# Kernel tuning notes

Measured on AMD Instinct MI355X. Metric: run time of the kernel, lower is better.

## Reference

```python
import jax, jax.numpy as jnp
import numpy as np

EPS = 1e-6  # torch F.cosine_similarity eps


def setup_inputs() -> dict:
    key = jax.random.key(0)
    k1, = jax.random.split(key, 1)
    N, M, D = 1024, 10, 768
    dvecs = jax.random.normal(k1, (N, M, D), dtype=jnp.float32)
    w = jnp.full((1,), 10.0, dtype=jnp.float32)   # init_w
    b = jnp.full((1,), -5.0, dtype=jnp.float32)   # init_b
    return {"dvecs": dvecs, "w": w, "b": b}


def _ge2e_softmax_loss(dvecs, w, b):
    N, M, D = dvecs.shape
    sums = jnp.sum(dvecs, axis=1)                      # (N, D)
    ctrds = sums / M                                   # full centroids
    excl = (sums[:, None, :] - dvecs) / (M - 1)        # (N, M, D) leave-one-out centroids

    dnorm = jnp.maximum(jnp.linalg.norm(dvecs, axis=-1), EPS)   # (N, M)
    cnorm = jnp.maximum(jnp.linalg.norm(ctrds, axis=-1), EPS)   # (N,)
    enorm = jnp.maximum(jnp.linalg.norm(excl, axis=-1), EPS)    # (N, M)

    # cosine sim of every utterance to every full centroid: (N, M, N)
    sim_all = jnp.einsum('nmd,kd->nmk', dvecs, ctrds) / (dnorm[:, :, None] * cnorm[None, None, :])
    # cosine sim of each utterance to its own excluded centroid: (N, M)
    sim_own = jnp.sum(dvecs * excl, axis=-1) / (dnorm * enorm)

    own_mask = jnp.eye(N, dtype=bool)[:, None, :]      # (N, 1, N)
    sim = jnp.where(own_mask, sim_own[:, :, None], sim_all)

    sim = sim * w[0] + b[0]
    losses = -jax.nn.log_softmax(sim, axis=2)          # (N, M, N)
    # pick entry [s, u, s] for each utterance
    own = jnp.take_along_axis(losses, jnp.broadcast_to(jnp.arange(N)[:, None, None], (N, M, 1)), axis=2)
    return jnp.sum(own)


def reference(dvecs, w, b):
    return _ge2e_softmax_loss(dvecs, w, b)
```

## Files before the change

### kernel.cpp

```cpp
#include <hip/hip_runtime.h>
#include <hip/hip_bf16.h>

#define EPS 1e-6f

typedef __attribute__((ext_vector_type(4))) float f32x4;

__device__ inline unsigned int pack_fp8x4(float x, float y, float z, float w) {
  int r = 0;
  r = __builtin_amdgcn_cvt_pk_fp8_f32(x, y, r, false);
  r = __builtin_amdgcn_cvt_pk_fp8_f32(z, w, r, true);
  return (unsigned int)r;
}

__global__ void __launch_bounds__(192) ge2e_pre(
    const float* __restrict__ dv, unsigned int* __restrict__ a8u,
    unsigned int* __restrict__ c8u, float* __restrict__ simown,
    float* __restrict__ rowsum, float* __restrict__ out) {
  const int n = blockIdx.x, t = threadIdx.x;
  if (n == 0 && t == 0) out[0] = 0.f;
  const float* base = dv + (size_t)n * 7680;
  float4 v[10];
  float4 s4 = make_float4(0.f, 0.f, 0.f, 0.f);
#pragma unroll
  for (int m = 0; m < 10; ++m) {
    v[m] = *reinterpret_cast<const float4*>(&base[m * 768 + 4 * t]);
    s4.x += v[m].x; s4.y += v[m].y; s4.z += v[m].z; s4.w += v[m].w;
  }
  float part[21];
#pragma unroll
  for (int m = 0; m < 10; ++m) {
    part[m]      = v[m].x * s4.x + v[m].y * s4.y + v[m].z * s4.z + v[m].w * s4.w;
    part[10 + m] = v[m].x * v[m].x + v[m].y * v[m].y + v[m].z * v[m].z + v[m].w * v[m].w;
  }
  part[20] = s4.x * s4.x + s4.y * s4.y + s4.z * s4.z + s4.w * s4.w;
#pragma unroll
  for (int k = 0; k < 21; ++k) {
#pragma unroll
    for (int off = 32; off >= 1; off >>= 1) part[k] += __shfl_xor(part[k], off);
  }
  __shared__ float red[3][21];
  __shared__ float bc[21];
  const int lane = t & 63, wid = t >> 6;
  if (lane == 0) {
#pragma unroll
    for (int k = 0; k < 21; ++k) red[wid][k] = part[k];
  }
  __syncthreads();
  if (t < 21) bc[t] = red[0][t] + red[1][t] + red[2][t];
  __syncthreads();
  const float ss = bc[20];
  const float rc = 1.0f / fmaxf(sqrtf(ss), 10.0f * EPS);
  c8u[n * 192 + t] = pack_fp8x4(s4.x * rc, s4.y * rc, s4.z * rc, s4.w * rc);
#pragma unroll
  for (int m = 0; m < 10; ++m) {
    float rd = 1.0f / fmaxf(sqrtf(bc[10 + m]), EPS);
    a8u[(size_t)(n * 10 + m) * 192 + t] =
        pack_fp8x4(v[m].x * rd, v[m].y * rd, v[m].z * rd, v[m].w * rd);
  }
  if (t < 10) {
    float dot = bc[t], sq = bc[10 + t];
    float dn = fmaxf(sqrtf(sq), EPS);
    float en = fmaxf(sqrtf(fmaxf(ss - 2.f * dot + sq, 0.f)) * (1.0f / 9.0f), EPS);
    simown[n * 10 + t] = ((dot - sq) * (1.0f / 9.0f)) / (dn * en);
    rowsum[n * 10 + t] = 0.f;
  }
}

__global__ void __launch_bounds__(256, 3) ge2e_gemm(
    const unsigned char* __restrict__ a8, const unsigned char* __restrict__ c8,
    const float* __restrict__ simown, const float* __restrict__ wp,
    float* __restrict__ rowsum) {
  __shared__ unsigned char As[2][2][128 * 32];
  __shared__ unsigned char Bs[2][2][128 * 32];
  const int t = threadIdx.x;
  const int lane = t & 63, wid = t >> 6;
  const int bx = blockIdx.x;
  const int wg = (bx & 7) * 80 + (bx >> 3);
  const int rb = wg >> 3, cb = wg & 7;
  const int row0 = rb * 128, col0 = cb * 128;
  const int wr = wid >> 1, wc = wid & 1;
  const int l15 = lane & 15, lg = lane >> 4;

  f32x4 acc[4][4];
#pragma unroll
  for (int i = 0; i < 4; ++i)
#pragma unroll
    for (int j = 0; j < 4; ++j) acc[i][j] = (f32x4){0.f, 0.f, 0.f, 0.f};

  auto STAGE = [&](int buf, int kk) {
#pragma unroll
    for (int jj = 0; jj < 2; ++jj) {
      const int s = wid * 2 + jj;
      const int c = s * 64 + lane;
      const int half = c >> 8, row = (c >> 1) & 127, k16 = c & 1;
      const unsigned char* srcA =
          a8 + (size_t)(row0 + row) * 768 + kk + half * 32 + k16 * 16;
      unsigned char* dstA = &As[buf][0][0] + s * 1024;
      __builtin_amdgcn_global_load_lds(
          (const __attribute__((address_space(1))) unsigned int*)srcA,
          (__attribute__((address_space(3))) unsigned int*)dstA, 16, 0, 0);
      const unsigned char* srcB =
          c8 + (size_t)(col0 + row) * 768 + kk + half * 32 + k16 * 16;
      unsigned char* dstB = &Bs[buf][0][0] + s * 1024;
      __builtin_amdgcn_global_load_lds(
          (const __attribute__((address_space(1))) unsigned int*)srcB,
          (__attribute__((address_space(3))) unsigned int*)dstB, 16, 0, 0);
    }
  };
  auto COMPUTE = [&](int buf) {
    long long af[4][2], bq[4][2];
#pragma unroll
    for (int i = 0; i < 4; ++i)
#pragma unroll
      for (int h = 0; h < 2; ++h)
        af[i][h] = *(const long long*)&As[buf][h][(wr * 64 + i * 16 + l15) * 32 + lg * 8];
#pragma unroll
    for (int j = 0; j < 4; ++j)
#pragma unroll
      for (int h = 0; h < 2; ++h)
        bq[j][h] = *(const long long*)&Bs[buf][h][(wc * 64 + j * 16 + l15) * 32 + lg * 8];
#pragma unroll
    for (int h = 0; h < 2; ++h)
#pragma unroll
      for (int i = 0; i < 4; ++i)
#pragma unroll
        for (int j = 0; j < 4; ++j)
          acc[i][j] = __builtin_amdgcn_mfma_f32_16x16x32_fp8_fp8(
              af[i][h], bq[j][h], acc[i][j], 0, 0, 0);
  };

  STAGE(0, 0);
  asm volatile("s_waitcnt vmcnt(0)" ::: "memory");
  __builtin_amdgcn_s_barrier();
  int cur = 0;
  for (int tt = 0; tt < 11; ++tt) {
    STAGE(cur ^ 1, (tt + 1) * 64);
    COMPUTE(cur);
    asm volatile("s_waitcnt vmcnt(0)" ::: "memory");
    __builtin_amdgcn_s_barrier();
    cur ^= 1;
  }
  COMPUTE(cur);

  const float wv = wp[0];
  const int R0 = row0 + wr * 64, C0 = col0 + wc * 64;
#pragma unroll
  for (int i = 0; i < 4; ++i) {
#pragma unroll
    for (int r = 0; r < 4; ++r) {
      const int grow = R0 + i * 16 + lg * 4 + r;
      const int ownc = grow / 10;
      float sm = 0.f;
#pragma unroll
      for (int j = 0; j < 4; ++j) {
        const int gcol = C0 + j * 16 + l15;
        float vv = wv * acc[i][j][r];
        if (gcol == ownc) vv = wv * simown[grow];
        sm += __expf(vv);
      }
#pragma unroll
      for (int off = 1; off < 16; off <<= 1) sm += __shfl_xor(sm, off, 16);
      if (l15 == 0) atomicAdd(&rowsum[grow], sm);
    }
  }
}

__global__ void __launch_bounds__(256) ge2e_final(
    const float* __restrict__ rowsum, const float* __restrict__ simown,
    const float* __restrict__ wp, float* __restrict__ out) {
  const int i = blockIdx.x * 256 + threadIdx.x;
  const float wv = wp[0];
  float loss = logf(rowsum[i]) - wv * simown[i];
#pragma unroll
  for (int off = 32; off >= 1; off >>= 1) loss += __shfl_xor(loss, off);
  __shared__ float red[4];
  const int lane = threadIdx.x & 63, wid = threadIdx.x >> 6;
  if (lane == 0) red[wid] = loss;
  __syncthreads();
  if (threadIdx.x == 0) atomicAdd(out, red[0] + red[1] + red[2] + red[3]);
}

extern "C" void kernel_launch(void* const* d_in, const int* in_sizes, int n_in,
                              void* d_out, int out_size, void* d_ws, size_t ws_size,
                              hipStream_t stream) {
  (void)in_sizes; (void)n_in; (void)out_size; (void)ws_size;
  const float* dv = (const float*)d_in[0];
  const float* wp = (const float*)d_in[1];

  unsigned char* a8 = (unsigned char*)d_ws;
  unsigned char* c8 = (unsigned char*)d_ws + 7864320;
  float* simown = (float*)((char*)d_ws + 8650752);
  float* rowsum = (float*)((char*)d_ws + 8691712);
  float* out = (float*)d_out;

  ge2e_pre<<<1024, 192, 0, stream>>>(dv, (unsigned int*)a8, (unsigned int*)c8,
                                     simown, rowsum, out);
  ge2e_gemm<<<640, 256, 0, stream>>>(a8, c8, simown, wp, rowsum);
  ge2e_final<<<40, 256, 0, stream>>>(rowsum, simown, wp, out);
}
```

Measured before the change: 47.36 us.

## Use 256x256 GEMM tiles with 8 waves, LDS swizzle, and interleaved staging

Grows the fp8 GEMM tile from 128x128 to 256x256 using 512-thread blocks (8 waves, each computing 128x64), cutting the grid to 160 blocks. An XOR swizzle on the LDS layout is meant to reduce bank conflicts. Loads for the next K-tile are split into half-steps interleaved with the MFMA groups, using partial vmcnt waits and setprio. This gives more data reuse per block, but 160 blocks may underfill the 256 CUs and each thread now holds more accumulators.

```diff
diff --git a/kernel.cpp b/kernel.cpp
--- a/kernel.cpp
+++ b/kernel.cpp
@@ -66,86 +66,126 @@
   }
 }
 
-__global__ void __launch_bounds__(256, 3) ge2e_gemm(
+__global__ void __launch_bounds__(512) ge2e_gemm(
     const unsigned char* __restrict__ a8, const unsigned char* __restrict__ c8,
     const float* __restrict__ simown, const float* __restrict__ wp,
     float* __restrict__ rowsum) {
-  __shared__ unsigned char As[2][2][128 * 32];
-  __shared__ unsigned char Bs[2][2][128 * 32];
+  __shared__ __align__(16) unsigned char As[2][2][8192];
+  __shared__ __align__(16) unsigned char Bs[2][2][8192];
   const int t = threadIdx.x;
   const int lane = t & 63, wid = t >> 6;
   const int bx = blockIdx.x;
-  const int wg = (bx & 7) * 80 + (bx >> 3);
-  const int rb = wg >> 3, cb = wg & 7;
-  const int row0 = rb * 128, col0 = cb * 128;
-  const int wr = wid >> 1, wc = wid & 1;
+  const int wg = (bx & 7) * 20 + (bx >> 3);
+  const int rb = wg >> 2, cb = wg & 3;
+  const int row0 = rb * 256, col0 = cb * 256;
+  const int wm = wid >> 2, wn = wid & 3;
   const int l15 = lane & 15, lg = lane >> 4;
 
-  f32x4 acc[4][4];
-#pragma unroll
-  for (int i = 0; i < 4; ++i)
+  f32x4 acc[8][4];
+#pragma unroll
+  for (int i = 0; i < 8; ++i)
 #pragma unroll
     for (int j = 0; j < 4; ++j) acc[i][j] = (f32x4){0.f, 0.f, 0.f, 0.f};
 
-  auto STAGE = [&](int buf, int kk) {
-#pragma unroll
-    for (int jj = 0; jj < 2; ++jj) {
-      const int s = wid * 2 + jj;
-      const int c = s * 64 + lane;
-      const int half = c >> 8, row = (c >> 1) & 127, k16 = c & 1;
-      const unsigned char* srcA =
-          a8 + (size_t)(row0 + row) * 768 + kk + half * 32 + k16 * 16;
-      unsigned char* dstA = &As[buf][0][0] + s * 1024;
-      __builtin_amdgcn_global_load_lds(
-          (const __attribute__((address_space(1))) unsigned int*)srcA,
-          (__attribute__((address_space(3))) unsigned int*)dstA, 16, 0, 0);
-      const unsigned char* srcB =
-          c8 + (size_t)(col0 + row) * 768 + kk + half * 32 + k16 * 16;
-      unsigned char* dstB = &Bs[buf][0][0] + s * 1024;
-      __builtin_amdgcn_global_load_lds(
-          (const __attribute__((address_space(1))) unsigned int*)srcB,
-          (__attribute__((address_space(3))) unsigned int*)dstB, 16, 0, 0);
-    }
-  };
-  auto COMPUTE = [&](int buf) {
-    long long af[4][2], bq[4][2];
-#pragma unroll
-    for (int i = 0; i < 4; ++i)
-#pragma unroll
-      for (int h = 0; h < 2; ++h)
-        af[i][h] = *(const long long*)&As[buf][h][(wr * 64 + i * 16 + l15) * 32 + lg * 8];
-#pragma unroll
-    for (int j = 0; j < 4; ++j)
-#pragma unroll
-      for (int h = 0; h < 2; ++h)
-        bq[j][h] = *(const long long*)&Bs[buf][h][(wc * 64 + j * 16 + l15) * 32 + lg * 8];
-#pragma unroll
-    for (int h = 0; h < 2; ++h)
-#pragma unroll
-      for (int i = 0; i < 4; ++i)
-#pragma unroll
-        for (int j = 0; j < 4; ++j)
-          acc[i][j] = __builtin_amdgcn_mfma_f32_16x16x32_fp8_fp8(
-              af[i][h], bq[j][h], acc[i][j], 0, 0, 0);
-  };
-
-  STAGE(0, 0);
-  asm volatile("s_waitcnt vmcnt(0)" ::: "memory");
-  __builtin_amdgcn_s_barrier();
-  int cur = 0;
+  const int chunk = wid * 64 + lane;
+  const int srow = chunk >> 1;
+  const int sk16 = (chunk & 1) ^ ((srow >> 2) & 1);
+  const unsigned char* aS = a8 + (size_t)(row0 + srow) * 768 + sk16 * 16;
+  const unsigned char* bS = c8 + (size_t)(col0 + srow) * 768 + sk16 * 16;
+
+  auto stageA = [&](int buf, int kh, int kb) {
+    __builtin_amdgcn_global_load_lds(
+        (const __attribute__((address_space(1))) unsigned int*)(aS + kb + kh * 32),
+        (__attribute__((address_space(3))) unsigned int*)&As[buf][kh][wid * 1024],
+        16, 0, 0);
+  };
+  auto stageB = [&](int buf, int kh, int kb) {
+    __builtin_amdgcn_global_load_lds(
+        (const __attribute__((address_space(1))) unsigned int*)(bS + kb + kh * 32),
+        (__attribute__((address_space(3))) unsigned int*)&Bs[buf][kh][wid * 1024],
+        16, 0, 0);
+  };
+  auto ldA = [&](int buf, int kh, int fr) -> long long {
+    const int r = wm * 128 + fr * 16 + l15;
+    return *(const long long*)&As[buf][kh]
+        [r * 32 + ((((lg >> 1) ^ ((r >> 2) & 1)) << 4) | ((lg & 1) << 3))];
+  };
+  auto ldB = [&](int buf, int kh, int fc) -> long long {
+    const int c = wn * 64 + fc * 16 + l15;
+    return *(const long long*)&Bs[buf][kh]
+        [c * 32 + ((((lg >> 1) ^ ((c >> 2) & 1)) << 4) | ((lg & 1) << 3))];
+  };
+
+#define MFMA_Q(RQ, AF, BF)                                                    \
+  do {                                                                        \
+    __builtin_amdgcn_s_setprio(1);                                            \
+    _Pragma("unroll") for (int i_ = 0; i_ < 4; ++i_)                          \
+    _Pragma("unroll") for (int j_ = 0; j_ < 4; ++j_)                          \
+      acc[(RQ) * 4 + i_][j_] = __builtin_amdgcn_mfma_f32_16x16x32_fp8_fp8(    \
+          AF[i_], BF[j_], acc[(RQ) * 4 + i_][j_], 0, 0, 0);                   \
+    __builtin_amdgcn_s_setprio(0);                                            \
+  } while (0)
+
+#define SYNC2 asm volatile("s_waitcnt vmcnt(2)" ::: "memory"); __builtin_amdgcn_s_barrier();
+#define SYNC0 asm volatile("s_waitcnt vmcnt(0)" ::: "memory"); __builtin_amdgcn_s_barrier();
+
+  stageA(0, 0, 0); stageB(0, 0, 0); stageA(0, 1, 0); stageB(0, 1, 0);
+
+  long long af[4], bf[4];
   for (int tt = 0; tt < 11; ++tt) {
-    STAGE(cur ^ 1, (tt + 1) * 64);
-    COMPUTE(cur);
-    asm volatile("s_waitcnt vmcnt(0)" ::: "memory");
-    __builtin_amdgcn_s_barrier();
-    cur ^= 1;
-  }
-  COMPUTE(cur);
+    const int b = tt & 1, nb = b ^ 1;
+    const int kn = (tt + 1) * 64;
+    SYNC2
+    stageA(nb, 0, kn);
+#pragma unroll
+    for (int j = 0; j < 4; ++j) bf[j] = ldB(b, 0, j);
+#pragma unroll
+    for (int i = 0; i < 4; ++i) af[i] = ldA(b, 0, i);
+    MFMA_Q(0, af, bf);
+    stageB(nb, 0, kn);
+#pragma unroll
+    for (int i = 0; i < 4; ++i) af[i] = ldA(b, 0, 4 + i);
+    MFMA_Q(1, af, bf);
+    SYNC2
+    stageA(nb, 1, kn);
+#pragma unroll
+    for (int j = 0; j < 4; ++j) bf[j] = ldB(b, 1, j);
+#pragma unroll
+    for (int i = 0; i < 4; ++i) af[i] = ldA(b, 1, i);
+    MFMA_Q(0, af, bf);
+    stageB(nb, 1, kn);
+#pragma unroll
+    for (int i = 0; i < 4; ++i) af[i] = ldA(b, 1, 4 + i);
+    MFMA_Q(1, af, bf);
+  }
+  {
+    SYNC2
+#pragma unroll
+    for (int j = 0; j < 4; ++j) bf[j] = ldB(1, 0, j);
+#pragma unroll
+    for (int i = 0; i < 4; ++i) af[i] = ldA(1, 0, i);
+    MFMA_Q(0, af, bf);
+#pragma unroll
+    for (int i = 0; i < 4; ++i) af[i] = ldA(1, 0, 4 + i);
+    MFMA_Q(1, af, bf);
+    SYNC0
+#pragma unroll
+    for (int j = 0; j < 4; ++j) bf[j] = ldB(1, 1, j);
+#pragma unroll
+    for (int i = 0; i < 4; ++i) af[i] = ldA(1, 1, i);
+    MFMA_Q(0, af, bf);
+#pragma unroll
+    for (int i = 0; i < 4; ++i) af[i] = ldA(1, 1, 4 + i);
+    MFMA_Q(1, af, bf);
+  }
+#undef MFMA_Q
+#undef SYNC2
+#undef SYNC0
 
   const float wv = wp[0];
-  const int R0 = row0 + wr * 64, C0 = col0 + wc * 64;
-#pragma unroll
-  for (int i = 0; i < 4; ++i) {
+  const int R0 = row0 + wm * 128, C0 = col0 + wn * 64;
+#pragma unroll
+  for (int i = 0; i < 8; ++i) {
 #pragma unroll
     for (int r = 0; r < 4; ++r) {
       const int grow = R0 + i * 16 + lg * 4 + r;
@@ -195,6 +235,6 @@
 
   ge2e_pre<<<1024, 192, 0, stream>>>(dv, (unsigned int*)a8, (unsigned int*)c8,
                                      simown, rowsum, out);
-  ge2e_gemm<<<640, 256, 0, stream>>>(a8, c8, simown, wp, rowsum);
+  ge2e_gemm<<<160, 512, 0, stream>>>(a8, c8, simown, wp, rowsum);
   ge2e_final<<<40, 256, 0, stream>>>(rowsum, simown, wp, out);
 }
```

After: 57.15 us. +20.7%, slower.
